# Performance work log

Hardware: AMD Instinct MI355X
Metric: run time of the kernel (lower is better)

The kernel has to match this reference:

```python
import jax, jax.numpy as jnp
import numpy as np
from jax import lax

L = 8
PATCH = 3
DIRS = [(0, 1), (1, 0), (1, 1), (1, -1)]


def _pair_indices():
    coords = np.arange(PATCH * PATCH)
    rr, cc = coords // PATCH, coords % PATCH
    i1s, i2s = [], []
    for dr, dc in DIRS:
        m = (rr + dr >= 0) & (rr + dr < PATCH) & (cc + dc >= 0) & (cc + dc < PATCH)
        i1s.append(coords[m])
        i2s.append((rr[m] + dr) * PATCH + (cc[m] + dc))
    return np.concatenate(i1s), np.concatenate(i2s)

_I1, _I2 = _pair_indices()


def conv_bn_silu(x, w, s, b, pad):
    # Conv2d(bias=False) + eval-mode BatchNorm folded into (s, b) + SiLU
    y = lax.conv_general_dilated(x, w, (1, 1), [(pad, pad), (pad, pad)],
                                 dimension_numbers=("NCHW", "OIHW", "NCHW"))
    y = y * s[None, :, None, None] + b[None, :, None, None]
    return jax.nn.silu(y)


def glcm_feats(x):
    B, C, H, W = x.shape
    pad = PATCH // 2
    xp = jnp.pad(x, ((0, 0), (0, 0), (pad, pad), (pad, pad)), mode="edge")
    # unfold: (B, C, 9, H, W)
    patches = jnp.stack([xp[:, :, i:i + H, j:j + W]
                         for i in range(PATCH) for j in range(PATCH)], axis=2)
    q = jnp.clip((patches * (L - 1)).astype(jnp.int32), 0, L - 1)
    q = q.reshape(B * C, PATCH * PATCH, H * W)
    # co-occurrence pair indices for all 4 directions, concatenated: (BC, K, HW)
    idx = q[:, _I1, :] * L + q[:, _I2, :]
    idx = idx.transpose(0, 2, 1)  # (BC, HW, K)
    # per-pixel local histogram over L*L bins (scatter-add)
    hist = jax.vmap(jax.vmap(
        lambda v: jnp.zeros((L * L,), x.dtype).at[v].add(1.0)))(idx)
    hist = hist / len(DIRS)  # reduce_mode='average'
    s = jnp.maximum(hist.sum(-1, keepdims=True), 1e-6)
    p = hist / s  # (BC, HW, L*L)
    li = jnp.arange(L, dtype=x.dtype)
    diff = li[:, None] - li[None, :]
    diff_sq = (diff ** 2).reshape(-1)
    abs_d = jnp.abs(diff).reshape(-1)
    contrast = (p * diff_sq).sum(-1)
    energy = (p * p).sum(-1)
    entropy = -(p * jnp.log(p + 1e-6)).sum(-1)
    homog = (p / (1.0 + abs_d)).sum(-1)
    f = jnp.stack([contrast, energy, entropy, homog], axis=-1)  # (BC, HW, 4)
    f = f.reshape(B, C, H * W, 4).mean(axis=1)  # average over channels
    return f.transpose(0, 2, 1).reshape(B, 4, H, W)


def setup_inputs() -> dict:
    key = jax.random.key(0)
    B, C, H, W = 4, 64, 80, 80
    c_, cb, c2 = 32, 16, 64
    ks = iter(jax.random.split(key, 20))
    x = jax.random.uniform(next(ks), (B, C, H, W), jnp.float32)

    def conv_p(cin, cout, ksz):
        w = jax.random.normal(next(ks), (cout, cin, ksz, ksz), jnp.float32) / np.sqrt(cin * ksz * ksz)
        s = jax.random.uniform(next(ks), (cout,), jnp.float32, 0.5, 1.5)
        b = jax.random.normal(next(ks), (cout,), jnp.float32) * 0.1
        return w, s, b

    cv1_w, cv1_s, cv1_b = conv_p(C + 4, c_, 1)
    cv2_w, cv2_s, cv2_b = conv_p(C + 4, c_, 1)
    m1_w, m1_s, m1_b = conv_p(c_, cb, 1)
    m2_w, m2_s, m2_b = conv_p(cb, c_, 3)
    cv3_w, cv3_s, cv3_b = conv_p(2 * c_, c2, 1)
    return dict(x=x, cv1_w=cv1_w, cv1_s=cv1_s, cv1_b=cv1_b,
                cv2_w=cv2_w, cv2_s=cv2_s, cv2_b=cv2_b,
                m1_w=m1_w, m1_s=m1_s, m1_b=m1_b,
                m2_w=m2_w, m2_s=m2_s, m2_b=m2_b,
                cv3_w=cv3_w, cv3_s=cv3_s, cv3_b=cv3_b)


def reference(x, cv1_w, cv1_s, cv1_b, cv2_w, cv2_s, cv2_b,
              m1_w, m1_s, m1_b, m2_w, m2_s, m2_b,
              cv3_w, cv3_s, cv3_b):
    g = glcm_feats(x)
    xc = jnp.concatenate([x, g], axis=1)  # (B, C+4, H, W)
    a = conv_bn_silu(xc, cv1_w, cv1_s, cv1_b, 0)
    y = conv_bn_silu(a, m1_w, m1_s, m1_b, 0)
    y = conv_bn_silu(y, m2_w, m2_s, m2_b, 1)
    a = a + y  # Bottleneck shortcut (c1 == c2)
    b = conv_bn_silu(xc, cv2_w, cv2_s, cv2_b, 0)
    return conv_bn_silu(jnp.concatenate([a, b], axis=1), cv3_w, cv3_s, cv3_b, 0)
```

## Files before the change

### kernel.cpp

```cpp
#include <hip/hip_runtime.h>
#include <math.h>

constexpr int B = 4, C = 64, H = 80, W = 80;
constexpr int HW = H * W;
constexpr int NPIX = B * HW;
constexpr int PXB = 16;

typedef unsigned u32;

static __device__ __forceinline__ float silu(float v) {
    float e = __expf(-v);
    return v * __builtin_amdgcn_rcpf(1.0f + e);
}

static __device__ __forceinline__ u32 pks(u32 a, u32 b){u32 d; asm("v_pk_sub_u16 %0,%1,%2":"=v"(d):"v"(a),"v"(b)); return d;}
static __device__ __forceinline__ u32 pka(u32 a, u32 b){u32 d; asm("v_pk_add_u16 %0,%1,%2":"=v"(d):"v"(a),"v"(b)); return d;}
static __device__ __forceinline__ u32 pkm(u32 a, u32 b){u32 d; asm("v_pk_mul_lo_u16 %0,%1,%2":"=v"(d):"v"(a),"v"(b)); return d;}
static __device__ __forceinline__ u32 pkmin(u32 a, u32 b){u32 d; asm("v_pk_min_u16 %0,%1,%2":"=v"(d):"v"(a),"v"(b)); return d;}
static __device__ __forceinline__ u32 pkmaxi(u32 a, u32 b){u32 d; asm("v_pk_max_i16 %0,%1,%2":"=v"(d):"v"(a),"v"(b)); return d;}
static __device__ __forceinline__ float cb0(u32 a){float f; asm("v_cvt_f32_ubyte0 %0,%1":"=v"(f):"v"(a)); return f;}
static __device__ __forceinline__ float cb2(u32 a){float f; asm("v_cvt_f32_ubyte2 %0,%1":"=v"(f):"v"(a)); return f;}

static __device__ __forceinline__ void ce(u32 &x, u32 &y) {
    u32 mn, mx;
    asm("v_pk_min_u16 %0, %2, %3\n\t"
        "v_pk_max_u16 %1, %2, %3"
        : "=&v"(mn), "=v"(mx) : "v"(x), "v"(y));
    x = mn; y = mx;
}

__global__ __launch_bounds__(512, 4) void glcm_stage1_kernel(
    const float* __restrict__ x,
    const float* __restrict__ w1, const float* __restrict__ s1, const float* __restrict__ b1,
    const float* __restrict__ w2, const float* __restrict__ s2, const float* __restrict__ b2,
    const float* __restrict__ wm1, const float* __restrict__ sm1, const float* __restrict__ bm1,
    float* __restrict__ a, float* __restrict__ bbuf, float* __restrict__ y16) {
    __shared__ u32 qcell[32][3][18];
    __shared__ __align__(16) float xs[PXB][72];
    __shared__ __align__(16) float ws1[32][68];
    __shared__ __align__(16) float ws2[32][68];
    __shared__ __align__(16) float wsm1[16][32];
    __shared__ float aT[PXB][33];
    __shared__ float red[8][PXB][4];

    const int t = threadIdx.x;
    const int p0g = blockIdx.x * PXB;
    const int bb  = p0g / HW;
    const int hw0 = p0g - bb * HW;
    const int h0  = hw0 / W;
    const int c0g = hw0 - h0 * W;

    {
        const float4* w1f = (const float4*)w1;
        const float4* w2f = (const float4*)w2;
        float4* s1f = (float4*)&ws1[0][0];
        float4* s2f = (float4*)&ws2[0][0];
        for (int e = t; e < 544; e += 512) { s1f[e] = w1f[e]; s2f[e] = w2f[e]; }
        if (t < 128) ((float4*)&wsm1[0][0])[t] = ((const float4*)wm1)[t];
    }
    for (int e = t; e < 32 * 3 * 18; e += 512) {
        const int grp = e / 54;
        const int rem = e - grp * 54;
        const int row = rem / 18;
        const int col = rem - row * 18;
        int gr = h0 + row - 1;  gr = gr < 0 ? 0 : (gr > H - 1 ? H - 1 : gr);
        int gc = c0g + col - 1; gc = gc < 0 ? 0 : (gc > W - 1 ? W - 1 : gc);
        const float v0 = x[((size_t)(bb * C + grp * 2)) * HW + gr * W + gc];
        const float v1 = x[((size_t)(bb * C + grp * 2 + 1)) * HW + gr * W + gc];
        int q0 = (int)(v0 * 7.0f); q0 = q0 < 0 ? 0 : (q0 > 7 ? 7 : q0);
        int q1 = (int)(v1 * 7.0f); q1 = q1 < 0 ? 0 : (q1 > 7 ? 7 : q1);
        qcell[grp][row][col] = (u32)q0 | ((u32)q1 << 16);
        if (row == 1 && col >= 1 && col <= 16) {
            xs[col - 1][grp * 2]     = v0;
            xs[col - 1][grp * 2 + 1] = v1;
        }
    }
    __syncthreads();

    const int pxl = t & 15;
    const int grp = t >> 4;
    u32 qpk[9];
    #pragma unroll
    for (int r = 0; r < 3; ++r)
        #pragma unroll
        for (int k = 0; k < 3; ++k)
            qpk[r * 3 + k] = qcell[grp][r][pxl + k];

    static constexpr int PA[20] = {0,1,3,4,6,7, 0,1,2,3,4,5, 0,1,3,4, 1,2,4,5};
    static constexpr int PB[20] = {1,2,4,5,7,8, 3,4,5,6,7,8, 4,5,7,8, 3,4,6,7};

    const u32 ONEpk = 0x00010001u, EIGHTpk = 0x00080008u;
    u32 cs = 0;
    float hsum = 0.f;
    u32 key[20];
    #pragma unroll
    for (int ai = 0; ai < 20; ++ai) {
        const u32 qa = qpk[PA[ai]], qb = qpk[PB[ai]];
        const u32 d = pks(qa, qb);
        cs = pka(cs, pkm(d, d));
        const u32 ad = pkmaxi(d, pks(0u, d));
        const u32 h1 = pka(ad, ONEpk);
        hsum += __builtin_amdgcn_rcpf(cb0(h1)) + __builtin_amdgcn_rcpf(cb2(h1));
        key[ai] = pka(pkm(qa, EIGHTpk), qb);
    }

    #pragma unroll
    for (int p = 1; p < 32; p <<= 1) {
        #pragma unroll
        for (int k = p; k >= 1; k >>= 1) {
            const int jm = k % p;
            #pragma unroll
            for (int lo = 0; lo < 20; ++lo) {
                const int hi = lo + k;
                if (hi < 20 && lo >= jm && ((lo - jm) % (2 * k)) < k &&
                    (lo / (2 * p)) == (hi / (2 * p))) {
                    ce(key[lo], key[hi]);
                }
            }
        }
    }

    u32 eq[20];
    #pragma unroll
    for (int ai = 1; ai < 20; ++ai)
        eq[ai] = pks(ONEpk, pkmin(pks(key[ai], key[ai - 1]), ONEpk));

    u32 pc = 0, ps = 0, pv[20];
    pv[0] = 0;
    #pragma unroll
    for (int ai = 1; ai < 20; ++ai) {
        pc = pkm(pka(pc, ONEpk), eq[ai]);
        pv[ai] = pc;
        ps = pka(ps, pc);
    }
    float pr0, pr1;
    {
        const u32 m = pka(pv[19], ONEpk);
        pr0 = cb0(m); pr1 = cb2(m);
    }
    u32 rc = 0;
    #pragma unroll
    for (int ai = 18; ai >= 0; --ai) {
        rc = pkm(pka(rc, ONEpk), eq[ai + 1]);
        const u32 m = pka(pka(pv[ai], rc), ONEpk);
        pr0 *= cb0(m); pr1 *= cb2(m);
    }

    const int csum = (int)(cs & 0xFFFFu) + (int)(cs >> 16);
    const int psum = (int)(ps & 0xFFFFu) + (int)(ps >> 16);
    const float lsum = __logf(pr0) + __logf(pr1);

    float fc = (float)csum * (1.f / 20.f);
    float fe = ((float)psum * 2.f + 40.f) * (1.f / 400.f);
    float fn = -(lsum + 40.f * -2.9957322736f) * (1.f / 20.f);
    float fh = hsum * (1.f / 20.f);

    fc += __shfl_xor(fc, 16); fe += __shfl_xor(fe, 16);
    fn += __shfl_xor(fn, 16); fh += __shfl_xor(fh, 16);
    fc += __shfl_xor(fc, 32); fe += __shfl_xor(fe, 32);
    fn += __shfl_xor(fn, 32); fh += __shfl_xor(fh, 32);
    const int wv = t >> 6;
    if ((t & 63) < 16) {
        red[wv][pxl][0] = fc; red[wv][pxl][1] = fe;
        red[wv][pxl][2] = fn; red[wv][pxl][3] = fh;
    }
    __syncthreads();
    if (t < 64) {
        const int p2 = t >> 2, f = t & 3;
        float s = 0.f;
        #pragma unroll
        for (int wq = 0; wq < 8; ++wq) s += red[wq][p2][f];
        xs[p2][64 + f] = s * (1.f / 64.f);
    }
    __syncthreads();

    {
        const int px = t & 15;
        const int oc = t >> 4;
        float acc1 = 0.f, acc2 = 0.f;
        #pragma unroll
        for (int k = 0; k < 17; ++k) {
            const float4 xv = *reinterpret_cast<const float4*>(&xs[px][k * 4]);
            const float4 wa = *reinterpret_cast<const float4*>(&ws1[oc][k * 4]);
            const float4 wb = *reinterpret_cast<const float4*>(&ws2[oc][k * 4]);
            acc1 += xv.x * wa.x + xv.y * wa.y + xv.z * wa.z + xv.w * wa.w;
            acc2 += xv.x * wb.x + xv.y * wb.y + xv.z * wb.z + xv.w * wb.w;
        }
        const int hw2 = hw0 + px;
        const float v1 = silu(acc1 * s1[oc] + b1[oc]);
        a[((size_t)(bb * 32 + oc)) * HW + hw2] = v1;
        aT[px][oc] = v1;
        bbuf[((size_t)(bb * 32 + oc)) * HW + hw2] = silu(acc2 * s2[oc] + b2[oc]);
    }
    __syncthreads();

    if (t < 256) {
        const int px = t & 15;
        const int oc = t >> 4;
        float acc = 0.f;
        #pragma unroll 8
        for (int ic = 0; ic < 32; ++ic)
            acc += aT[px][ic] * wsm1[oc][ic];
        y16[((size_t)(bb * 16 + oc)) * HW + hw0 + px] = silu(acc * sm1[oc] + bm1[oc]);
    }
}

__global__ __launch_bounds__(512) void m2cv3_kernel(
    const float* __restrict__ y16, const float* __restrict__ a,
    const float* __restrict__ bbuf,
    const float* __restrict__ wm2, const float* __restrict__ sm2, const float* __restrict__ bm2,
    const float* __restrict__ wc, const float* __restrict__ sc, const float* __restrict__ bc,
    float* __restrict__ out) {
    __shared__ float ys[16][4][82];
    __shared__ float a2[32][64];
    __shared__ float bs[32][64];
    const int t = threadIdx.x;
    const int p0 = blockIdx.x * 64;
    const int bi = p0 / HW;
    const int hw0 = p0 - bi * HW;
    const int h0 = hw0 / W;

    const float* yb = y16 + (size_t)(bi * 16) * HW;
    for (int e = t; e < 16 * 4 * 82; e += 512) {
        const int ch = e / 328;
        const int rem = e - ch * 328;
        const int row = rem / 82;
        const int col = rem - row * 82;
        const int r = h0 - 1 + row;
        const int c = col - 1;
        float v = 0.f;
        if ((unsigned)r < (unsigned)H && (unsigned)c < (unsigned)W)
            v = yb[(size_t)ch * HW + r * W + c];
        ys[ch][row][col] = v;
    }
    for (int e = t; e < 32 * 64; e += 512) {
        const int ic = e >> 6, px = e & 63;
        bs[ic][px] = bbuf[((size_t)(bi * 32 + ic)) * HW + hw0 + px];
    }
    __syncthreads();

    const int lane = t & 63;
    const int wv = __builtin_amdgcn_readfirstlane(t >> 6);
    const int hw = hw0 + lane;
    const int h = hw / W;
    const int w = hw - h * W;
    const int lr = h - h0;
    const int oc0 = wv * 4;

    float acc[4] = {0.f, 0.f, 0.f, 0.f};
    #pragma unroll 2
    for (int ic = 0; ic < 16; ++ic) {
        #pragma unroll
        for (int ky = 0; ky < 3; ++ky) {
            #pragma unroll
            for (int kx = 0; kx < 3; ++kx) {
                const float v = ys[ic][lr + ky][w + kx];
                const int tap = ic * 9 + ky * 3 + kx;
                #pragma unroll
                for (int j = 0; j < 4; ++j)
                    acc[j] += v * wm2[(oc0 + j) * 144 + tap];
            }
        }
    }
    #pragma unroll
    for (int j = 0; j < 4; ++j) {
        const int oc = oc0 + j;
        a2[oc][lane] = a[((size_t)(bi * 32 + oc)) * HW + hw]
                     + silu(acc[j] * sm2[oc] + bm2[oc]);
    }
    __syncthreads();
    const int oc3 = wv * 8;
    float c_[8] = {0.f, 0.f, 0.f, 0.f, 0.f, 0.f, 0.f, 0.f};
    #pragma unroll 4
    for (int ic = 0; ic < 32; ++ic) {
        const float av = a2[ic][lane];
        const float bv = bs[ic][lane];
        #pragma unroll
        for (int j = 0; j < 8; ++j) {
            c_[j] += av * wc[(oc3 + j) * 64 + ic];
            c_[j] += bv * wc[(oc3 + j) * 64 + 32 + ic];
        }
    }
    #pragma unroll
    for (int j = 0; j < 8; ++j) {
        const int oc = oc3 + j;
        out[((size_t)(bi * 64 + oc)) * HW + hw] = silu(c_[j] * sc[oc] + bc[oc]);
    }
}

extern "C" void kernel_launch(void* const* d_in, const int* in_sizes, int n_in,
                              void* d_out, int out_size, void* d_ws, size_t ws_size,
                              hipStream_t stream) {
    const float* x    = (const float*)d_in[0];
    const float* cv1w = (const float*)d_in[1];
    const float* cv1s = (const float*)d_in[2];
    const float* cv1b = (const float*)d_in[3];
    const float* cv2w = (const float*)d_in[4];
    const float* cv2s = (const float*)d_in[5];
    const float* cv2b = (const float*)d_in[6];
    const float* m1w  = (const float*)d_in[7];
    const float* m1s  = (const float*)d_in[8];
    const float* m1b  = (const float*)d_in[9];
    const float* m2w  = (const float*)d_in[10];
    const float* m2s  = (const float*)d_in[11];
    const float* m2b  = (const float*)d_in[12];
    const float* cv3w = (const float*)d_in[13];
    const float* cv3s = (const float*)d_in[14];
    const float* cv3b = (const float*)d_in[15];

    float* ws   = (float*)d_ws;
    float* a    = ws;
    float* bbuf = ws + 819200;
    float* y16  = ws + 1638400;

    glcm_stage1_kernel<<<NPIX / PXB, 512, 0, stream>>>(
        x, cv1w, cv1s, cv1b, cv2w, cv2s, cv2b, m1w, m1s, m1b, a, bbuf, y16);
    m2cv3_kernel<<<NPIX / 64, 512, 0, stream>>>(y16, a, bbuf, m2w, m2s, m2b,
                                                cv3w, cv3s, cv3b, (float*)d_out);
}
```

Before: 61.49 us.

## Use packed FP32 FMA in stage-1 convs, merge reciprocals, raise occupancy bound

Replaces the scalar float4 dot products in the fused 1x1 convolutions with v_pk_fma_f32 on float pairs, halving FMA instruction count. Merges the two per-pair reciprocals in the homogeneity sum into one (a+b)/(a*b) form. Raises launch_bounds min blocks to 8, changes the shared-memory layout (flattened qcell with stride 80, padded rows) and switches to a scalar wsm1 load. The tighter register cap may cause spills, and the row padding changes LDS bank patterns.

```diff
diff --git a/kernel.cpp b/kernel.cpp
--- a/kernel.cpp
+++ b/kernel.cpp
@@ -7,6 +7,7 @@
 constexpr int PXB = 16;
 
 typedef unsigned u32;
+typedef float f32x2 __attribute__((ext_vector_type(2)));
 
 static __device__ __forceinline__ float silu(float v) {
     float e = __expf(-v);
@@ -29,18 +30,22 @@
     x = mn; y = mx;
 }
 
-__global__ __launch_bounds__(512, 4) void glcm_stage1_kernel(
+static __device__ __forceinline__ void pkfma(f32x2 &acc, f32x2 a, f32x2 b){
+    asm("v_pk_fma_f32 %0, %1, %2, %0" : "+v"(acc) : "v"(a), "v"(b));
+}
+
+__global__ __launch_bounds__(512, 8) void glcm_stage1_kernel(
     const float* __restrict__ x,
     const float* __restrict__ w1, const float* __restrict__ s1, const float* __restrict__ b1,
     const float* __restrict__ w2, const float* __restrict__ s2, const float* __restrict__ b2,
     const float* __restrict__ wm1, const float* __restrict__ sm1, const float* __restrict__ bm1,
     float* __restrict__ a, float* __restrict__ bbuf, float* __restrict__ y16) {
-    __shared__ u32 qcell[32][3][18];
-    __shared__ __align__(16) float xs[PXB][72];
+    __shared__ u32 qcellF[32 * 80];
+    __shared__ __align__(16) float xs[PXB][76];
     __shared__ __align__(16) float ws1[32][68];
     __shared__ __align__(16) float ws2[32][68];
-    __shared__ __align__(16) float wsm1[16][32];
-    __shared__ float aT[PXB][33];
+    __shared__ __align__(16) float wsm1[16][34];
+    __shared__ __align__(16) float aT[PXB][34];
     __shared__ float red[8][PXB][4];
 
     const int t = threadIdx.x;
@@ -56,7 +61,7 @@
         float4* s1f = (float4*)&ws1[0][0];
         float4* s2f = (float4*)&ws2[0][0];
         for (int e = t; e < 544; e += 512) { s1f[e] = w1f[e]; s2f[e] = w2f[e]; }
-        if (t < 128) ((float4*)&wsm1[0][0])[t] = ((const float4*)wm1)[t];
+        wsm1[t >> 5][t & 31] = wm1[t];
     }
     for (int e = t; e < 32 * 3 * 18; e += 512) {
         const int grp = e / 54;
@@ -69,7 +74,7 @@
         const float v1 = x[((size_t)(bb * C + grp * 2 + 1)) * HW + gr * W + gc];
         int q0 = (int)(v0 * 7.0f); q0 = q0 < 0 ? 0 : (q0 > 7 ? 7 : q0);
         int q1 = (int)(v1 * 7.0f); q1 = q1 < 0 ? 0 : (q1 > 7 ? 7 : q1);
-        qcell[grp][row][col] = (u32)q0 | ((u32)q1 << 16);
+        qcellF[grp * 80 + row * 18 + col] = (u32)q0 | ((u32)q1 << 16);
         if (row == 1 && col >= 1 && col <= 16) {
             xs[col - 1][grp * 2]     = v0;
             xs[col - 1][grp * 2 + 1] = v1;
@@ -84,7 +89,7 @@
     for (int r = 0; r < 3; ++r)
         #pragma unroll
         for (int k = 0; k < 3; ++k)
-            qpk[r * 3 + k] = qcell[grp][r][pxl + k];
+            qpk[r * 3 + k] = qcellF[grp * 80 + r * 18 + pxl + k];
 
     static constexpr int PA[20] = {0,1,3,4,6,7, 0,1,2,3,4,5, 0,1,3,4, 1,2,4,5};
     static constexpr int PB[20] = {1,2,4,5,7,8, 3,4,5,6,7,8, 4,5,7,8, 3,4,6,7};
@@ -100,7 +105,11 @@
         cs = pka(cs, pkm(d, d));
         const u32 ad = pkmaxi(d, pks(0u, d));
         const u32 h1 = pka(ad, ONEpk);
-        hsum += __builtin_amdgcn_rcpf(cb0(h1)) + __builtin_amdgcn_rcpf(cb2(h1));
+        const u32 lo = h1 & 0xFFFFu;
+        const u32 hi = h1 >> 16;
+        const float pf = (float)(lo * hi);
+        const float sf = (float)(lo + hi);
+        hsum += sf * __builtin_amdgcn_rcpf(pf);
         key[ai] = pka(pkm(qa, EIGHTpk), qb);
     }
 
@@ -177,15 +186,18 @@
     {
         const int px = t & 15;
         const int oc = t >> 4;
-        float acc1 = 0.f, acc2 = 0.f;
-        #pragma unroll
-        for (int k = 0; k < 17; ++k) {
-            const float4 xv = *reinterpret_cast<const float4*>(&xs[px][k * 4]);
-            const float4 wa = *reinterpret_cast<const float4*>(&ws1[oc][k * 4]);
-            const float4 wb = *reinterpret_cast<const float4*>(&ws2[oc][k * 4]);
-            acc1 += xv.x * wa.x + xv.y * wa.y + xv.z * wa.z + xv.w * wa.w;
-            acc2 += xv.x * wb.x + xv.y * wb.y + xv.z * wb.z + xv.w * wb.w;
-        }
+        const f32x2* xv2 = (const f32x2*)&xs[px][0];
+        const f32x2* w1v = (const f32x2*)&ws1[oc][0];
+        const f32x2* w2v = (const f32x2*)&ws2[oc][0];
+        f32x2 A1 = {0.f, 0.f}, A2 = {0.f, 0.f};
+        #pragma unroll
+        for (int k = 0; k < 34; ++k) {
+            const f32x2 xv = xv2[k];
+            pkfma(A1, xv, w1v[k]);
+            pkfma(A2, xv, w2v[k]);
+        }
+        const float acc1 = A1.x + A1.y;
+        const float acc2 = A2.x + A2.y;
         const int hw2 = hw0 + px;
         const float v1 = silu(acc1 * s1[oc] + b1[oc]);
         a[((size_t)(bb * 32 + oc)) * HW + hw2] = v1;
@@ -197,10 +209,12 @@
     if (t < 256) {
         const int px = t & 15;
         const int oc = t >> 4;
-        float acc = 0.f;
-        #pragma unroll 8
-        for (int ic = 0; ic < 32; ++ic)
-            acc += aT[px][ic] * wsm1[oc][ic];
+        const f32x2* at2 = (const f32x2*)&aT[px][0];
+        const f32x2* wmv = (const f32x2*)&wsm1[oc][0];
+        f32x2 A = {0.f, 0.f};
+        #pragma unroll
+        for (int k = 0; k < 16; ++k) pkfma(A, at2[k], wmv[k]);
+        const float acc = A.x + A.y;
         y16[((size_t)(bb * 16 + oc)) * HW + hw0 + px] = silu(acc * sm1[oc] + bm1[oc]);
     }
 }
```

Result: slower. 63.78 us (+3.7%).
